# Performance work log

Measured on AMD Instinct MI355X. Metric: run time of the kernel, lower is better.

Reference implementation:

```python
import jax, jax.numpy as jnp
import numpy as np

EPS = 1e-5
H = 16  # num_heads


def _ln(x, s, b):
    m = x.mean(-1, keepdims=True)
    v = x.var(-1, keepdims=True)
    return (x - m) / jnp.sqrt(v + EPS) * s + b


def _gru_gate(x, y, W, U, bg):
    # W, U: [3, D, D] stacked (Wr, Wz, Wg) / (Ur, Uz, Ug); torch Linear: a @ W.T
    r = jax.nn.sigmoid(y @ W[0].T + x @ U[0].T)
    z = jax.nn.sigmoid(y @ W[1].T + x @ U[1].T - bg)
    h = jnp.tanh(y @ W[2].T + (r * x) @ U[2].T)
    return (1.0 - z) * x + z * h


def setup_inputs() -> dict:
    N, L, D = 4, 1024, 1024
    hs = D // H
    rng = jax.random.key(0)
    ks = iter(jax.random.split(rng, 24))

    def xav(shape):
        sc = float(np.sqrt(2.0 / (shape[-1] + shape[-2])))
        return jax.random.normal(next(ks), shape, jnp.float32) * sc

    inp = {
        'value': jax.random.normal(next(ks), (N, L, D), jnp.float32),
        'key': jax.random.normal(next(ks), (N, L, D), jnp.float32),
        'query': jax.random.normal(next(ks), (N, L, D), jnp.float32),
        'mask': jax.random.randint(next(ks), (N, L), 0, 2).astype(jnp.int32),
        # shared-head QKV projections (head_size x head_size)
        'wq': xav((hs, hs)), 'wk': xav((hs, hs)), 'wv': xav((hs, hs)),
        'w_out': xav((D, D)), 'b_out': jnp.zeros((D,), jnp.float32),
        'fc_w': xav((D, D)), 'fc_b': jnp.zeros((D,), jnp.float32),
        'ln1_s': jnp.ones((D,), jnp.float32), 'ln1_b': jnp.zeros((D,), jnp.float32),
        'lnkv_s': jnp.ones((D,), jnp.float32), 'lnkv_b': jnp.zeros((D,), jnp.float32),
        'ln2_s': jnp.ones((D,), jnp.float32), 'ln2_b': jnp.zeros((D,), jnp.float32),
        'g1_W': xav((3, D, D)), 'g1_U': xav((3, D, D)), 'g1_bg': jnp.full((D,), 2.0, jnp.float32),
        'g2_W': xav((3, D, D)), 'g2_U': xav((3, D, D)), 'g2_bg': jnp.full((D,), 2.0, jnp.float32),
    }
    return inp


def reference(value, key, query, mask, wq, wk, wv, w_out, b_out, fc_w, fc_b,
              ln1_s, ln1_b, lnkv_s, lnkv_b, ln2_s, ln2_b,
              g1_W, g1_U, g1_bg, g2_W, g2_U, g2_bg):
    N, L, D = query.shape
    hs = D // H
    # pre-LN: query normed with norm1, value normed with norm_kv; key := normed value
    q_ = _ln(query, ln1_s, ln1_b)
    v_ = _ln(value, lnkv_s, lnkv_b)
    k_ = v_
    # shared per-head projections: [N, L, H, hs] @ W.T
    qh = q_.reshape(N, L, H, hs) @ wq.T
    kh = k_.reshape(N, L, H, hs) @ wk.T
    vh = v_.reshape(N, L, H, hs) @ wv.T
    energy = jnp.einsum('nqhd,nkhd->nhqk', qh, kh)
    energy = jnp.where(mask[:, None, None, :] == 0, jnp.float32(-1e20), energy)
    # NOTE: original scales by sqrt(embed_dim), not sqrt(head_size)
    attn = jax.nn.softmax(energy / jnp.sqrt(jnp.float32(D)), axis=-1)
    o = jnp.einsum('nhqk,nkhd->nqhd', attn, vh).reshape(N, L, D) @ w_out.T + b_out
    # GRU-gated residuals (GTrXL)
    h = _gru_gate(query, o, g1_W, g1_U, g1_bg)
    h_ = _ln(h, ln2_s, ln2_b)
    f = jax.nn.relu(h_ @ fc_w.T + fc_b)
    out = _gru_gate(h, f, g2_W, g2_U, g2_bg)
    return out, attn
```

## Files before the change

### kernel.cpp

```cpp
#include <hip/hip_runtime.h>
#include <cstdint>
#include <cstddef>

#define N_ 4
#define L_ 1024
#define D_ 1024
#define H_ 16
#define HS_ 64
#define M_ (N_*L_)
#define DD_ (D_*D_)
#define MD_ ((size_t)M_*D_)

typedef unsigned short u16;
typedef __bf16 b16x8 __attribute__((ext_vector_type(8)));
typedef float f32x4 __attribute__((ext_vector_type(4)));

__device__ __forceinline__ float sigmoidf_(float x) { return 1.0f / (1.0f + __expf(-x)); }
__device__ __forceinline__ u16 f2bf(float f) {
    union { float f; uint32_t u; } c; c.f = f;
    uint32_t u = c.u;
    u += 0x7fffu + ((u >> 16) & 1u);
    return (u16)(u >> 16);
}

__device__ __forceinline__ void gl_lds16(const void* g, void* l) {
    auto gp = reinterpret_cast<const __attribute__((address_space(1))) unsigned int*>(
        reinterpret_cast<uintptr_t>(g));
    auto lp = reinterpret_cast<__attribute__((address_space(3))) unsigned int*>(
        reinterpret_cast<uintptr_t>(l));
    __builtin_amdgcn_global_load_lds(gp, lp, 16, 0, 0);
}

__global__ __launch_bounds__(256) void prep_weights_kernel(
    const float* __restrict__ w_out, const float* __restrict__ fc_w,
    const float* __restrict__ wq, const float* __restrict__ wk, const float* __restrict__ wv,
    const float* __restrict__ g1W, const float* __restrict__ g1U,
    const float* __restrict__ g2W, const float* __restrict__ g2U,
    const float* __restrict__ query, u16* __restrict__ Xq,
    u16* __restrict__ ws0) {
    u16* Wop = ws0;
    u16* Wfc = ws0 + (size_t)DD_;
    u16* WQKV = ws0 + 2 * (size_t)DD_;
    u16* G1rz = WQKV + 16384;
    u16* G1h = G1rz + 4 * (size_t)DD_;
    u16* G2rz = G1h + 2 * (size_t)DD_;
    u16* G2h = G2rz + 4 * (size_t)DD_;
    int b = blockIdx.x, t = threadIdx.x;
    const float* src; u16* dst; size_t si, di;
    if (b < 512) {
        size_t f = (size_t)b * 2048 + t * 8; src = w_out; si = f; dst = Wop; di = f;
    } else if (b < 1024) {
        size_t f = (size_t)(b - 512) * 2048 + t * 8; src = fc_w; si = f; dst = Wfc; di = f;
    } else if (b < 1030) {
        size_t f = (size_t)(b - 1024) * 2048 + t * 8;
        int which = (int)(f >> 12); size_t off = f & 4095;
        src = which == 0 ? wq : (which == 1 ? wk : wv); si = off; dst = WQKV; di = f;
    } else if (b < 3078) {
        size_t f = (size_t)(b - 1030) * 2048 + t * 8;
        size_t row = f >> 11, k = f & 2047; size_t n2 = (row >= 1024) ? 1 : 0;
        src = (k < 1024) ? (g1W + n2 * DD_) : (g1U + n2 * DD_);
        si = (row & 1023) * 1024 + (k & 1023); dst = G1rz; di = f;
    } else if (b < 4102) {
        size_t f = (size_t)(b - 3078) * 2048 + t * 8;
        size_t row = f >> 11, k = f & 2047;
        src = (k < 1024) ? (g1W + 2 * (size_t)DD_) : (g1U + 2 * (size_t)DD_);
        si = row * 1024 + (k & 1023); dst = G1h; di = f;
    } else if (b < 6150) {
        size_t f = (size_t)(b - 4102) * 2048 + t * 8;
        size_t row = f >> 11, k = f & 2047; size_t n2 = (row >= 1024) ? 1 : 0;
        src = (k < 1024) ? (g2W + n2 * DD_) : (g2U + n2 * DD_);
        si = (row & 1023) * 1024 + (k & 1023); dst = G2rz; di = f;
    } else if (b < 7174) {
        size_t f = (size_t)(b - 6150) * 2048 + t * 8;
        size_t row = f >> 11, k = f & 2047;
        src = (k < 1024) ? (g2W + 2 * (size_t)DD_) : (g2U + 2 * (size_t)DD_);
        si = row * 1024 + (k & 1023); dst = G2h; di = f;
    } else {
        size_t f = (size_t)(b - 7174) * 2048 + t * 8;
        src = query; si = f; dst = Xq; di = f;
    }
    float4 a = *(const float4*)&src[si];
    float4 b4 = *(const float4*)&src[si + 4];
    u16 o[8] = { f2bf(a.x), f2bf(a.y), f2bf(a.z), f2bf(a.w),
                 f2bf(b4.x), f2bf(b4.y), f2bf(b4.z), f2bf(b4.w) };
    *(uint4*)&dst[di] = *(uint4*)o;
}

__global__ __launch_bounds__(256) void ln2in1_kernel(const float* __restrict__ x0, u16* __restrict__ y0,
                                                     const float* __restrict__ sc0, const float* __restrict__ bi0,
                                                     const float* __restrict__ x1, u16* __restrict__ y1,
                                                     const float* __restrict__ sc1, const float* __restrict__ bi1) {
    int row = blockIdx.x;
    const float* x = blockIdx.y ? x1 : x0;
    u16* y = blockIdx.y ? y1 : y0;
    const float* sc = blockIdx.y ? sc1 : sc0;
    const float* bi = blockIdx.y ? bi1 : bi0;
    const float* xr = x + (size_t)row * D_;
    int t = threadIdx.x;
    float4 v = *(const float4*)&xr[t * 4];
    float s = v.x + v.y + v.z + v.w;
    float q = v.x * v.x + v.y * v.y + v.z * v.z + v.w * v.w;
#pragma unroll
    for (int o = 32; o > 0; o >>= 1) { s += __shfl_xor(s, o); q += __shfl_xor(q, o); }
    __shared__ float ss[4], sq[4];
    int w = t >> 6;
    if ((t & 63) == 0) { ss[w] = s; sq[w] = q; }
    __syncthreads();
    s = ss[0] + ss[1] + ss[2] + ss[3];
    q = sq[0] + sq[1] + sq[2] + sq[3];
    float mean = s * (1.0f / D_);
    float var = q * (1.0f / D_) - mean * mean;
    float inv = rsqrtf(var + 1e-5f);
    float4 sv = *(const float4*)&sc[t * 4];
    float4 bv = *(const float4*)&bi[t * 4];
    u16 ov[4] = { f2bf((v.x - mean) * inv * sv.x + bv.x),
                  f2bf((v.y - mean) * inv * sv.y + bv.y),
                  f2bf((v.z - mean) * inv * sv.z + bv.z),
                  f2bf((v.w - mean) * inv * sv.w + bv.w) };
    *(ushort4*)&y[(size_t)row * D_ + t * 4] = *(ushort4*)ov;
}

__global__ __launch_bounds__(256) void ln_kernel(const float* __restrict__ x, u16* __restrict__ y,
                                                 const float* __restrict__ sc, const float* __restrict__ bi) {
    int row = blockIdx.x;
    const float* xr = x + (size_t)row * D_;
    int t = threadIdx.x;
    float4 v = *(const float4*)&xr[t * 4];
    float s = v.x + v.y + v.z + v.w;
    float q = v.x * v.x + v.y * v.y + v.z * v.z + v.w * v.w;
#pragma unroll
    for (int o = 32; o > 0; o >>= 1) { s += __shfl_xor(s, o); q += __shfl_xor(q, o); }
    __shared__ float ss[4], sq[4];
    int w = t >> 6;
    if ((t & 63) == 0) { ss[w] = s; sq[w] = q; }
    __syncthreads();
    s = ss[0] + ss[1] + ss[2] + ss[3];
    q = sq[0] + sq[1] + sq[2] + sq[3];
    float mean = s * (1.0f / D_);
    float var = q * (1.0f / D_) - mean * mean;
    float inv = rsqrtf(var + 1e-5f);
    float4 sv = *(const float4*)&sc[t * 4];
    float4 bv = *(const float4*)&bi[t * 4];
    u16 ov[4] = { f2bf((v.x - mean) * inv * sv.x + bv.x),
                  f2bf((v.y - mean) * inv * sv.y + bv.y),
                  f2bf((v.z - mean) * inv * sv.z + bv.z),
                  f2bf((v.w - mean) * inv * sv.w + bv.w) };
    *(ushort4*)&y[(size_t)row * D_ + t * 4] = *(ushort4*)ov;
}

__global__ __launch_bounds__(256) void proj_mfma_kernel(const u16* __restrict__ qbf,
                                                        const u16* __restrict__ vbf,
                                                        const u16* __restrict__ wqkv,
                                                        u16* __restrict__ qh, u16* __restrict__ kh,
                                                        u16* __restrict__ vt) {
    int t = threadIdx.x, w = t >> 6, l = t & 63;
    int lr = l & 15, lg = l >> 4;
    int rb = blockIdx.x, h = blockIdx.y;
    int n = rb >> 3, lbase = (rb & 7) * 128;
    const u16* wqp = wqkv;
    const u16* wkp = wqkv + 4096;
    const u16* wvp = wqkv + 8192;
    b16x8 wqf[4][2], wkf[4][2], wvf[4][2];
#pragma unroll
    for (int dt = 0; dt < 4; ++dt)
#pragma unroll
        for (int ks = 0; ks < 2; ++ks) {
            int a = (dt * 16 + lr) * 64 + ks * 32 + lg * 8;
            wqf[dt][ks] = *(const b16x8*)&wqp[a];
            wkf[dt][ks] = *(const b16x8*)&wkp[a];
            wvf[dt][ks] = *(const b16x8*)&wvp[a];
        }
#pragma unroll
    for (int rr = 0; rr < 2; ++rr) {
        int rt = w * 2 + rr;
        size_t grow = (size_t)(n * 1024 + lbase + rt * 16 + lr);
        b16x8 aq[2], av[2];
#pragma unroll
        for (int ks = 0; ks < 2; ++ks) {
            aq[ks] = *(const b16x8*)&qbf[grow * D_ + h * 64 + ks * 32 + lg * 8];
            av[ks] = *(const b16x8*)&vbf[grow * D_ + h * 64 + ks * 32 + lg * 8];
        }
#pragma unroll
        for (int dt = 0; dt < 4; ++dt) {
            f32x4 cq = (f32x4){0.f, 0.f, 0.f, 0.f};
            f32x4 ck = (f32x4){0.f, 0.f, 0.f, 0.f};
            f32x4 cv = (f32x4){0.f, 0.f, 0.f, 0.f};
            cq = __builtin_amdgcn_mfma_f32_16x16x32_bf16(aq[0], wqf[dt][0], cq, 0, 0, 0);
            cq = __builtin_amdgcn_mfma_f32_16x16x32_bf16(aq[1], wqf[dt][1], cq, 0, 0, 0);
            ck = __builtin_amdgcn_mfma_f32_16x16x32_bf16(av[0], wkf[dt][0], ck, 0, 0, 0);
            ck = __builtin_amdgcn_mfma_f32_16x16x32_bf16(av[1], wkf[dt][1], ck, 0, 0, 0);
            cv = __builtin_amdgcn_mfma_f32_16x16x32_bf16(wvf[dt][0], av[0], cv, 0, 0, 0);
            cv = __builtin_amdgcn_mfma_f32_16x16x32_bf16(wvf[dt][1], av[1], cv, 0, 0, 0);
#pragma unroll
            for (int r = 0; r < 4; ++r) {
                size_t orow = (size_t)(n * 1024 + lbase + rt * 16 + lg * 4 + r);
                qh[orow * D_ + h * 64 + dt * 16 + lr] = f2bf(cq[r]);
                kh[orow * D_ + h * 64 + dt * 16 + lr] = f2bf(ck[r]);
                vt[((size_t)(n * H_ + h) * 64 + dt * 16 + lg * 4 + r) * L_ + lbase + rt * 16 + lr] = f2bf(cv[r]);
            }
        }
    }
}

#define PSTR 1032
__global__ __launch_bounds__(512, 4) void qk_pv_kernel(const u16* __restrict__ qh,
                                                       const u16* __restrict__ kh,
                                                       const u16* __restrict__ vt,
                                                       const int* __restrict__ mask,
                                                       float* __restrict__ attn,
                                                       u16* __restrict__ obf) {
    __shared__ u16 P_lds[32 * PSTR];
    __shared__ float redA[32][4];
    __shared__ float redB[32][4];
    int t = threadIdx.x;
    int w = t >> 6, l = t & 63;
    int qsub = w & 1, kq = w >> 1;
    int q0 = blockIdx.x * 32;
    int h = blockIdx.y, n = blockIdx.z;
    int lr = l & 15, lg = l >> 4;

    size_t qrow = ((size_t)(n * L_ + q0 + qsub * 16 + lr) * H_ + h) * HS_;
    b16x8 aq0 = *(const b16x8*)&qh[qrow + lg * 8];
    b16x8 aq1 = *(const b16x8*)&qh[qrow + 32 + lg * 8];

    f32x4 c[16];
#pragma unroll
    for (int i = 0; i < 16; ++i) c[i] = (f32x4){0.f, 0.f, 0.f, 0.f};

    size_t kbase = ((size_t)(n * L_ + kq * 256 + lr) * H_ + h) * HS_ + lg * 8;
#pragma unroll
    for (int kt = 0; kt < 16; ++kt) {
        const u16* kp = &kh[kbase + (size_t)kt * 16 * D_];
        b16x8 bk0 = *(const b16x8*)&kp[0];
        b16x8 bk1 = *(const b16x8*)&kp[32];
        c[kt] = __builtin_amdgcn_mfma_f32_16x16x32_bf16(aq0, bk0, c[kt], 0, 0, 0);
        c[kt] = __builtin_amdgcn_mfma_f32_16x16x32_bf16(aq1, bk1, c[kt], 0, 0, 0);
    }

    const float scl = 0.03125f;
    int kcol = kq * 256 + lr;
    float rowmax[4] = { -1e30f, -1e30f, -1e30f, -1e30f };
#pragma unroll
    for (int kt = 0; kt < 16; ++kt) {
        int mk = mask[n * L_ + kcol + kt * 16];
#pragma unroll
        for (int r = 0; r < 4; ++r) {
            float s = (mk != 0) ? c[kt][r] * scl : -1e20f;
            c[kt][r] = s;
            rowmax[r] = fmaxf(rowmax[r], s);
        }
    }
#pragma unroll
    for (int o = 8; o > 0; o >>= 1)
#pragma unroll
        for (int r = 0; r < 4; ++r) rowmax[r] = fmaxf(rowmax[r], __shfl_xor(rowmax[r], o));

    int qrow4 = qsub * 16 + lg * 4;
    if (lr == 0) {
#pragma unroll
        for (int r = 0; r < 4; ++r) redA[qrow4 + r][kq] = rowmax[r];
    }
    __syncthreads();
#pragma unroll
    for (int r = 0; r < 4; ++r)
        rowmax[r] = fmaxf(fmaxf(redA[qrow4 + r][0], redA[qrow4 + r][1]),
                          fmaxf(redA[qrow4 + r][2], redA[qrow4 + r][3]));
    float rowsum[4] = { 0.f, 0.f, 0.f, 0.f };
#pragma unroll
    for (int kt = 0; kt < 16; ++kt)
#pragma unroll
        for (int r = 0; r < 4; ++r) {
            float e = __expf(c[kt][r] - rowmax[r]);
            c[kt][r] = e;
            rowsum[r] += e;
        }
#pragma unroll
    for (int o = 8; o > 0; o >>= 1)
#pragma unroll
        for (int r = 0; r < 4; ++r) rowsum[r] += __shfl_xor(rowsum[r], o);
    if (lr == 0) {
#pragma unroll
        for (int r = 0; r < 4; ++r) redB[qrow4 + r][kq] = rowsum[r];
    }
    __syncthreads();
    float inv[4];
#pragma unroll
    for (int r = 0; r < 4; ++r)
        inv[r] = 1.0f / (redB[qrow4 + r][0] + redB[qrow4 + r][1] +
                         redB[qrow4 + r][2] + redB[qrow4 + r][3]);

    float* ap = attn + ((size_t)((n * H_ + h) * L_) + q0 + qrow4) * L_ + kcol;
#pragma unroll
    for (int kt = 0; kt < 16; ++kt)
#pragma unroll
        for (int r = 0; r < 4; ++r) {
            float val = c[kt][r] * inv[r];
            ap[(size_t)r * L_ + kt * 16] = val;
            P_lds[(size_t)(qrow4 + r) * PSTR + kcol + kt * 16] = f2bf(val);
        }
    __syncthreads();

    int dg = kq;
    const u16* vb = vt + ((size_t)(n * H_ + h) * 64 + dg * 16 + lr) * L_;
    const u16* prow = &P_lds[(size_t)(qsub * 16 + lr) * PSTR];
    f32x4 acc = (f32x4){0.f, 0.f, 0.f, 0.f};
#pragma unroll
    for (int ks = 0; ks < 32; ++ks) {
        b16x8 a = *(const b16x8*)&prow[ks * 32 + lg * 8];
        b16x8 b = *(const b16x8*)&vb[ks * 32 + lg * 8];
        acc = __builtin_amdgcn_mfma_f32_16x16x32_bf16(a, b, acc, 0, 0, 0);
    }
#pragma unroll
    for (int r = 0; r < 4; ++r) {
        size_t q = (size_t)(n * L_ + q0 + qsub * 16 + lg * 4 + r);
        obf[q * D_ + h * 64 + dg * 16 + lr] = f2bf(acc[r]);
    }
}

template<int MODE, int RELU, int WRH, int DEPTH>
__global__ __launch_bounds__(512, 4) void gemm_fused_kernel(const u16* __restrict__ A0,
                                                            const u16* __restrict__ A1h,
                                                            const u16* __restrict__ Bw,
                                                            const float* __restrict__ bias,
                                                            const float* __restrict__ xf,
                                                            float* __restrict__ Z,
                                                            u16* __restrict__ Cbf,
                                                            float* __restrict__ outf,
                                                            int K) {
    __shared__ u16 As[DEPTH][128 * 64];
    __shared__ u16 Bs[DEPTH][128 * 64];
    int t = threadIdx.x, w = t >> 6, l = t & 63;
    int wr = w & 3, wc = w >> 2;
    int gx = gridDim.x, gy = gridDim.y;
    int flat = blockIdx.y * gx + blockIdx.x;
    int ppx = gy >> 3;
    int idx = flat >> 3;
    int by = (flat & 7) * ppx + (idx >> 5);
    int bx = idx & 31;
    int m0 = bx * 128, n0 = by * 128;
    int fr = l & 15, fq = l >> 4;
    int srow = l >> 3;
    int gc8 = (l & 7) ^ (srow & 7);
    const u16* Bbase = Bw + (size_t)n0 * K;

    f32x4 acc[2][4];
#pragma unroll
    for (int i = 0; i < 2; ++i)
#pragma unroll
        for (int j = 0; j < 4; ++j) acc[i][j] = (f32x4){0.f, 0.f, 0.f, 0.f};

    auto STAGE = [&](int buf, int kk) {
        const u16* Asrc = (MODE == 0 || kk < 1024) ? A0 : A1h;
        int kc = kk & 1023;
#pragma unroll
        for (int i = 0; i < 2; ++i) {
            int r0 = (i * 8 + w) * 8;
            gl_lds16(&Asrc[(size_t)(m0 + r0 + srow) * 1024 + kc + gc8 * 8], &As[buf][r0 * 64]);
            gl_lds16(&Bbase[(size_t)(r0 + srow) * K + kk + gc8 * 8], &Bs[buf][r0 * 64]);
        }
    };

    const int NT = K >> 6;

    auto COMPUTE = [&](int cur) {
#pragma unroll
        for (int ks = 0; ks < 2; ++ks) {
            b16x8 af[2], bf[4];
#pragma unroll
            for (int i = 0; i < 2; ++i) {
                int row = wr * 32 + i * 16 + fr;
                af[i] = *(const b16x8*)&As[cur][row * 64 + (((ks * 4 + fq) ^ (fr & 7)) * 8)];
            }
#pragma unroll
            for (int j = 0; j < 4; ++j) {
                int row = wc * 64 + j * 16 + fr;
                bf[j] = *(const b16x8*)&Bs[cur][row * 64 + (((ks * 4 + fq) ^ (fr & 7)) * 8)];
            }
#pragma unroll
            for (int i = 0; i < 2; ++i)
#pragma unroll
                for (int j = 0; j < 4; ++j)
                    acc[i][j] = __builtin_amdgcn_mfma_f32_16x16x32_bf16(af[i], bf[j], acc[i][j], 0, 0, 0);
        }
    };

    if (DEPTH == 2) {
        STAGE(0, 0);
        for (int kt = 0; kt < NT; ++kt) {
            int cur = kt & 1;
            if (kt + 1 < NT) {
                STAGE(cur ^ 1, (kt + 1) << 6);
                asm volatile("s_waitcnt vmcnt(4)" ::: "memory");
            } else {
                asm volatile("s_waitcnt vmcnt(0)" ::: "memory");
            }
            __builtin_amdgcn_s_barrier();
            COMPUTE(cur);
            asm volatile("s_waitcnt lgkmcnt(0)" ::: "memory");
            __builtin_amdgcn_s_barrier();
        }
    } else {
        STAGE(0, 0);
        STAGE(1, 64);
        int cur = 0;
        for (int kt = 0; kt < NT; ++kt) {
            if (kt + 1 < NT) {
                asm volatile("s_waitcnt vmcnt(4)" ::: "memory");
            } else {
                asm volatile("s_waitcnt vmcnt(0)" ::: "memory");
            }
            __builtin_amdgcn_s_barrier();
            if (kt + 2 < NT) STAGE((kt + 2) % 3, (kt + 2) << 6);
            COMPUTE(cur);
            cur = (cur + 1) % 3;
        }
    }

#pragma unroll
    for (int i = 0; i < 2; ++i) {
#pragma unroll
        for (int j = 0; j < 4; ++j) {
            int row = m0 + wr * 32 + i * 16 + fq * 4;
            int col = n0 + wc * 64 + j * 16 + fr;
            int c1 = col & 1023;
#pragma unroll
            for (int r = 0; r < 4; ++r) {
                float v = acc[i][j][r];
                size_t off = (size_t)(row + r) * 1024 + c1;
                if (MODE == 0) {
                    v += bias[col];
                    if (RELU) v = fmaxf(v, 0.f);
                    Cbf[off] = f2bf(v);
                } else if (MODE == 1) {
                    if (col < 1024) Cbf[off] = f2bf(sigmoidf_(v) * xf[off]);
                    else            Z[off] = sigmoidf_(v - bias[c1]);
                } else {
                    float z = Z[off];
                    float o = (1.f - z) * xf[off] + z * tanhf(v);
                    outf[off] = o;
                    if (WRH) Cbf[off] = f2bf(o);
                }
            }
        }
    }
}

extern "C" void kernel_launch(void* const* d_in, const int* in_sizes, int n_in,
                              void* d_out, int out_size, void* d_ws, size_t ws_size,
                              hipStream_t stream) {
    const float* value = (const float*)d_in[0];
    const float* query = (const float*)d_in[2];
    const int* mask = (const int*)d_in[3];
    const float* wq = (const float*)d_in[4];
    const float* wk = (const float*)d_in[5];
    const float* wv = (const float*)d_in[6];
    const float* w_out = (const float*)d_in[7];
    const float* b_out = (const float*)d_in[8];
    const float* fc_w = (const float*)d_in[9];
    const float* fc_b = (const float*)d_in[10];
    const float* ln1_s = (const float*)d_in[11];
    const float* ln1_b = (const float*)d_in[12];
    const float* lnkv_s = (const float*)d_in[13];
    const float* lnkv_b = (const float*)d_in[14];
    const float* ln2_s = (const float*)d_in[15];
    const float* ln2_b = (const float*)d_in[16];
    const float* g1_W = (const float*)d_in[17];
    const float* g1_U = (const float*)d_in[18];
    const float* g1_bg = (const float*)d_in[19];
    const float* g2_W = (const float*)d_in[20];
    const float* g2_U = (const float*)d_in[21];
    const float* g2_bg = (const float*)d_in[22];

    float* out_f = (float*)d_out;
    float* attn_f = out_f + MD_;
    float* OutH = out_f;

    u16* WS = (u16*)d_ws;
    u16* Wop = WS;
    u16* Wfc = WS + (size_t)DD_;
    u16* WQKV = WS + 2 * (size_t)DD_;
    u16* G1rz = WQKV + 16384;
    u16* G1h  = G1rz + 4 * (size_t)DD_;
    u16* G2rz = G1h + 2 * (size_t)DD_;
    u16* G2h  = G2rz + 4 * (size_t)DD_;
    u16* Y    = G2h + 2 * (size_t)DD_;
    u16* Xq   = Y + MD_;
    u16* T1   = Xq + MD_;
    u16* Hb   = T1 + MD_;
    u16* F    = Hb + MD_;
    u16* QH   = F + MD_;
    u16* KH   = QH + MD_;
    u16* VT   = KH + MD_;
    u16* OBF  = VT + MD_;
    u16* LNQ  = OBF + MD_;
    u16* LNV  = LNQ + MD_;
    u16* LN2  = LNV + MD_;
    float* Z  = (float*)(LN2 + MD_);

    dim3 grid_n1024(M_ / 128, 8);
    dim3 grid_n2048(M_ / 128, 16);

    prep_weights_kernel<<<9222, 256, 0, stream>>>(w_out, fc_w, wq, wk, wv,
                                                  g1_W, g1_U, g2_W, g2_U, query, Xq, WS);

    ln2in1_kernel<<<dim3(M_, 2), 256, 0, stream>>>(query, LNQ, ln1_s, ln1_b,
                                                   value, LNV, lnkv_s, lnkv_b);
    proj_mfma_kernel<<<dim3(32, 16), 256, 0, stream>>>(LNQ, LNV, WQKV, QH, KH, VT);
    qk_pv_kernel<<<dim3(L_ / 32, H_, N_), 512, 0, stream>>>(QH, KH, VT, mask, attn_f, OBF);
    gemm_fused_kernel<0, 0, 0, 3><<<grid_n1024, 512, 0, stream>>>(OBF, nullptr, Wop, b_out,
                                                                  nullptr, nullptr, Y, nullptr, 1024);
    gemm_fused_kernel<1, 0, 0, 2><<<grid_n2048, 512, 0, stream>>>(Y, Xq, G1rz, g1_bg,
                                                                  query, Z, T1, nullptr, 2048);
    gemm_fused_kernel<2, 0, 1, 3><<<grid_n1024, 512, 0, stream>>>(Y, T1, G1h, nullptr,
                                                                  query, Z, Hb, OutH, 2048);
    ln_kernel<<<M_, 256, 0, stream>>>(OutH, LN2, ln2_s, ln2_b);
    gemm_fused_kernel<0, 1, 0, 3><<<grid_n1024, 512, 0, stream>>>(LN2, nullptr, Wfc, fc_b,
                                                                  nullptr, nullptr, F, nullptr, 1024);
    gemm_fused_kernel<1, 0, 0, 2><<<grid_n2048, 512, 0, stream>>>(F, Hb, G2rz, g2_bg,
                                                                  OutH, Z, T1, nullptr, 2048);
    gemm_fused_kernel<2, 0, 0, 3><<<grid_n1024, 512, 0, stream>>>(F, T1, G2h, nullptr,
                                                                  OutH, Z, nullptr, out_f, 2048);
}
```

Measured before the change: 410.4 us.

## Use streaming cache hints on GEMM A loads and attn stores, drop triple buffering

The A-operand global-to-LDS loads in the fused GEMM now carry a cache-policy aux bit, and the fp32 attention-probability stores use nontemporal stores. Both are meant to keep streamed activations and the large attn output from evicting the reused weight panels from cache. The triple-buffered GEMM pipeline is removed, so every GEMM runs the double-buffered loop with two barriers per k-step. The grid becomes a 1D launch with the same XCD-aware panel mapping, which drops the 2D index arithmetic. Going back to double buffering may expose more load latency but lowers LDS use per block.

```diff
diff --git a/kernel.cpp b/kernel.cpp
--- a/kernel.cpp
+++ b/kernel.cpp
@@ -23,12 +23,13 @@
     return (u16)(u >> 16);
 }
 
+template<int AUX>
 __device__ __forceinline__ void gl_lds16(const void* g, void* l) {
     auto gp = reinterpret_cast<const __attribute__((address_space(1))) unsigned int*>(
         reinterpret_cast<uintptr_t>(g));
     auto lp = reinterpret_cast<__attribute__((address_space(3))) unsigned int*>(
         reinterpret_cast<uintptr_t>(l));
-    __builtin_amdgcn_global_load_lds(gp, lp, 16, 0, 0);
+    __builtin_amdgcn_global_load_lds(gp, lp, 16, 0, AUX);
 }
 
 __global__ __launch_bounds__(256) void prep_weights_kernel(
@@ -295,7 +296,7 @@
 #pragma unroll
         for (int r = 0; r < 4; ++r) {
             float val = c[kt][r] * inv[r];
-            ap[(size_t)r * L_ + kt * 16] = val;
+            __builtin_nontemporal_store(val, &ap[(size_t)r * L_ + kt * 16]);
             P_lds[(size_t)(qrow4 + r) * PSTR + kcol + kt * 16] = f2bf(val);
         }
     __syncthreads();
@@ -317,7 +318,7 @@
     }
 }
 
-template<int MODE, int RELU, int WRH, int DEPTH>
+template<int MODE, int RELU, int WRH>
 __global__ __launch_bounds__(512, 4) void gemm_fused_kernel(const u16* __restrict__ A0,
                                                             const u16* __restrict__ A1h,
                                                             const u16* __restrict__ Bw,
@@ -327,17 +328,17 @@
                                                             u16* __restrict__ Cbf,
                                                             float* __restrict__ outf,
                                                             int K) {
-    __shared__ u16 As[DEPTH][128 * 64];
-    __shared__ u16 Bs[DEPTH][128 * 64];
+    __shared__ u16 As[2][128 * 64];
+    __shared__ u16 Bs[2][128 * 64];
     int t = threadIdx.x, w = t >> 6, l = t & 63;
     int wr = w & 3, wc = w >> 2;
-    int gx = gridDim.x, gy = gridDim.y;
-    int flat = blockIdx.y * gx + blockIdx.x;
-    int ppx = gy >> 3;
-    int idx = flat >> 3;
-    int by = (flat & 7) * ppx + (idx >> 5);
-    int bx = idx & 31;
-    int m0 = bx * 128, n0 = by * 128;
+    int flat = blockIdx.x;
+    int xcd = flat & 7, idx = flat >> 3;
+    int NP = gridDim.x >> 5;
+    int ppx = NP >> 3;
+    int panel = xcd * ppx + (idx >> 5);
+    int mchunk = idx & 31;
+    int m0 = mchunk * 128, n0 = panel * 128;
     int fr = l & 15, fq = l >> 4;
     int srow = l >> 3;
     int gc8 = (l & 7) ^ (srow & 7);
@@ -355,14 +356,21 @@
 #pragma unroll
         for (int i = 0; i < 2; ++i) {
             int r0 = (i * 8 + w) * 8;
-            gl_lds16(&Asrc[(size_t)(m0 + r0 + srow) * 1024 + kc + gc8 * 8], &As[buf][r0 * 64]);
-            gl_lds16(&Bbase[(size_t)(r0 + srow) * K + kk + gc8 * 8], &Bs[buf][r0 * 64]);
+            gl_lds16<2>(&Asrc[(size_t)(m0 + r0 + srow) * 1024 + kc + gc8 * 8], &As[buf][r0 * 64]);
+            gl_lds16<0>(&Bbase[(size_t)(r0 + srow) * K + kk + gc8 * 8], &Bs[buf][r0 * 64]);
         }
     };
-
+    STAGE(0, 0);
     const int NT = K >> 6;
-
-    auto COMPUTE = [&](int cur) {
+    for (int kt = 0; kt < NT; ++kt) {
+        int cur = kt & 1;
+        if (kt + 1 < NT) {
+            STAGE(cur ^ 1, (kt + 1) << 6);
+            asm volatile("s_waitcnt vmcnt(4)" ::: "memory");
+        } else {
+            asm volatile("s_waitcnt vmcnt(0)" ::: "memory");
+        }
+        __builtin_amdgcn_s_barrier();
 #pragma unroll
         for (int ks = 0; ks < 2; ++ks) {
             b16x8 af[2], bf[4];
@@ -382,38 +390,8 @@
                 for (int j = 0; j < 4; ++j)
                     acc[i][j] = __builtin_amdgcn_mfma_f32_16x16x32_bf16(af[i], bf[j], acc[i][j], 0, 0, 0);
         }
-    };
-
-    if (DEPTH == 2) {
-        STAGE(0, 0);
-        for (int kt = 0; kt < NT; ++kt) {
-            int cur = kt & 1;
-            if (kt + 1 < NT) {
-                STAGE(cur ^ 1, (kt + 1) << 6);
-                asm volatile("s_waitcnt vmcnt(4)" ::: "memory");
-            } else {
-                asm volatile("s_waitcnt vmcnt(0)" ::: "memory");
-            }
-            __builtin_amdgcn_s_barrier();
-            COMPUTE(cur);
-            asm volatile("s_waitcnt lgkmcnt(0)" ::: "memory");
-            __builtin_amdgcn_s_barrier();
-        }
-    } else {
-        STAGE(0, 0);
-        STAGE(1, 64);
-        int cur = 0;
-        for (int kt = 0; kt < NT; ++kt) {
-            if (kt + 1 < NT) {
-                asm volatile("s_waitcnt vmcnt(4)" ::: "memory");
-            } else {
-                asm volatile("s_waitcnt vmcnt(0)" ::: "memory");
-            }
-            __builtin_amdgcn_s_barrier();
-            if (kt + 2 < NT) STAGE((kt + 2) % 3, (kt + 2) << 6);
-            COMPUTE(cur);
-            cur = (cur + 1) % 3;
-        }
+        asm volatile("s_waitcnt lgkmcnt(0)" ::: "memory");
+        __builtin_amdgcn_s_barrier();
     }
 
 #pragma unroll
@@ -497,8 +475,8 @@
     u16* LN2  = LNV + MD_;
     float* Z  = (float*)(LN2 + MD_);
 
-    dim3 grid_n1024(M_ / 128, 8);
-    dim3 grid_n2048(M_ / 128, 16);
+    dim3 grid_n1024(256);
+    dim3 grid_n2048(512);
 
     prep_weights_kernel<<<9222, 256, 0, stream>>>(w_out, fc_w, wq, wk, wv,
                                                   g1_W, g1_U, g2_W, g2_U, query, Xq, WS);
@@ -507,17 +485,17 @@
                                                    value, LNV, lnkv_s, lnkv_b);
     proj_mfma_kernel<<<dim3(32, 16), 256, 0, stream>>>(LNQ, LNV, WQKV, QH, KH, VT);
     qk_pv_kernel<<<dim3(L_ / 32, H_, N_), 512, 0, stream>>>(QH, KH, VT, mask, attn_f, OBF);
-    gemm_fused_kernel<0, 0, 0, 3><<<grid_n1024, 512, 0, stream>>>(OBF, nullptr, Wop, b_out,
-                                                                  nullptr, nullptr, Y, nullptr, 1024);
-    gemm_fused_kernel<1, 0, 0, 2><<<grid_n2048, 512, 0, stream>>>(Y, Xq, G1rz, g1_bg,
-                                                                  query, Z, T1, nullptr, 2048);
-    gemm_fused_kernel<2, 0, 1, 3><<<grid_n1024, 512, 0, stream>>>(Y, T1, G1h, nullptr,
-                                                                  query, Z, Hb, OutH, 2048);
+    gemm_fused_kernel<0, 0, 0><<<grid_n1024, 512, 0, stream>>>(OBF, nullptr, Wop, b_out,
+                                                               nullptr, nullptr, Y, nullptr, 1024);
+    gemm_fused_kernel<1, 0, 0><<<grid_n2048, 512, 0, stream>>>(Y, Xq, G1rz, g1_bg,
+                                                               query, Z, T1, nullptr, 2048);
+    gemm_fused_kernel<2, 0, 1><<<grid_n1024, 512, 0, stream>>>(Y, T1, G1h, nullptr,
+                                                               query, Z, Hb, OutH, 2048);
     ln_kernel<<<M_, 256, 0, stream>>>(OutH, LN2, ln2_s, ln2_b);
-    gemm_fused_kernel<0, 1, 0, 3><<<grid_n1024, 512, 0, stream>>>(LN2, nullptr, Wfc, fc_b,
-                                                                  nullptr, nullptr, F, nullptr, 1024);
-    gemm_fused_kernel<1, 0, 0, 2><<<grid_n2048, 512, 0, stream>>>(F, Hb, G2rz, g2_bg,
-                                                                  OutH, Z, T1, nullptr, 2048);
-    gemm_fused_kernel<2, 0, 0, 3><<<grid_n1024, 512, 0, stream>>>(F, T1, G2h, nullptr,
-                                                                  OutH, Z, nullptr, out_f, 2048);
-}
+    gemm_fused_kernel<0, 1, 0><<<grid_n1024, 512, 0, stream>>>(LN2, nullptr, Wfc, fc_b,
+                                                               nullptr, nullptr, F, nullptr, 1024);
+    gemm_fused_kernel<1, 0, 0><<<grid_n2048, 512, 0, stream>>>(F, Hb, G2rz, g2_bg,
+                                                               OutH, Z, T1, nullptr, 2048);
+    gemm_fused_kernel<2, 0, 0><<<grid_n1024, 512, 0, stream>>>(F, T1, G2h, nullptr,
+                                                               OutH, Z, nullptr, out_f, 2048);
+}
```

Measured after the change: 446.8 us. 1.09x slower.
